# Optimization experiments

Measured on AMD Instinct MI355X. Metric: run time of the kernel, lower is better.

Reference implementation:

```python
import jax, jax.numpy as jnp
import numpy as np

B, D = 16384, 512


def setup_inputs() -> dict:
    key = jax.random.key(0)
    ks = jax.random.split(key, 7)
    s1 = 1.0 / np.sqrt(D + 1)
    s2 = 1.0 / np.sqrt(2 * D + 1)
    return {
        "t": jax.random.uniform(ks[0], (1,), dtype=jnp.float32),
        "z": jax.random.normal(ks[1], (B, D), dtype=jnp.float32),
        "logp_z": jnp.zeros((B, 1), dtype=jnp.float32),
        "W1": jax.random.normal(ks[2], (2 * D, D + 1), dtype=jnp.float32) * s1,
        "b1": jax.random.normal(ks[3], (2 * D,), dtype=jnp.float32) * s1,
        "W2": jax.random.normal(ks[4], (D, 2 * D + 1), dtype=jnp.float32) * s2,
        "b2": jax.random.normal(ks[5], (D,), dtype=jnp.float32) * s2,
    }


def reference(t, z, logp_z, W1, b1, W2, b2):
    # CNF dynamics: dz/dt = fc2(concat(relu(fc1(concat(z, t))), t))
    batch = z.shape[0]
    tt = jnp.full((batch, 1), t[0], dtype=z.dtype)
    x = jnp.concatenate([z, tt], axis=1)            # [B, D+1]
    h_pre = x @ W1.T + b1                           # [B, 2D]
    h = jax.nn.relu(h_pre)
    x2 = jnp.concatenate([h, tt], axis=1)           # [B, 2D+1]
    dz_dt = x2 @ W2.T + b2                          # [B, D]

    # Exact Jacobian trace of linear-relu-linear block (closed form of the
    # per-dim autograd loop in trace_df_dz):
    #   tr J = sum_h relu'(h_pre[:,h]) * (sum_i W2[i,h] * W1[h,i])
    W2h = W2[:, : 2 * D]                            # drop time column, [D, 2D]
    W1z = W1[:, :D]                                 # drop time column, [2D, D]
    c = jnp.sum(W2h.T * W1z, axis=1)                # [2D]
    mask = (h_pre > 0).astype(z.dtype)              # relu'
    trace = mask @ c                                # [B]
    dlogp_z_dt = -trace[:, None]                    # [B, 1]
    return dz_dt, dlogp_z_dt
```

## Files before the change

### kernel.cpp

```cpp
#include <hip/hip_runtime.h>
#include <stdint.h>

#define B_   16384
#define D_   512
#define N1_  1024
#define K1_  512
#define N2_  512
#define K2_  1024

#define DELTA     4e-3f
#define LIST_CAP  (1u << 21)
#define LCAP      1024u

typedef _Float16 f16x8 __attribute__((ext_vector_type(8)));
typedef _Float16 f16x4 __attribute__((ext_vector_type(4)));
typedef float    f32x4 __attribute__((ext_vector_type(4)));

#define MFMA(a, b, c) __builtin_amdgcn_mfma_f32_16x16x32_f16(a, b, c, 0, 0, 0)

__global__ __launch_bounds__(256) void prep_w(
    const float* __restrict__ t,
    const float* __restrict__ W1, const float* __restrict__ b1,
    const float* __restrict__ W2, const float* __restrict__ b2,
    _Float16* __restrict__ wp,
    float* __restrict__ bias1, float* __restrict__ bias2,
    float* __restrict__ cvec, uint32_t* __restrict__ counter) {
  int blk = blockIdx.x, tid = threadIdx.x;
  if (blk < 512) {
    int idx = blk * 256 + tid;
    int g = idx >> 11, rem = idx & 2047;
    int w = rem >> 8, nt = (rem >> 6) & 3, lane = rem & 63;
    int m16 = lane & 15, q = lane >> 4;
    int ch = g >> 5, ph = g & 31;
    const float* src;
    float scale;
    if (ph < 16) {
      int col = ch * 512 + w * 64 + nt * 16 + m16;
      int k = ph * 32 + q * 8;
      src = W1 + (size_t)col * 513 + k;
      scale = 64.f;
    } else {
      int col = w * 64 + nt * 16 + m16;
      int k = ch * 512 + (ph - 16) * 32 + q * 8;
      src = W2 + (size_t)col * 1025 + k;
      scale = 1.f;
    }
    f16x8 hv;
    #pragma unroll
    for (int e = 0; e < 8; ++e) hv[e] = (_Float16)(src[e] * scale);
    *(f16x8*)(wp + (size_t)idx * 8) = hv;
  } else if (blk < 516) {
    int j = (blk - 512) * 256 + tid;
    float t0 = t[0];
    bias1[j] = b1[j] + t0 * W1[(size_t)j * 513 + 512];
    if (j < 512) bias2[j] = b2[j] + t0 * W2[(size_t)j * 1025 + 1024];
    if (j == 0) *counter = 0;
  } else {
    int wave = tid >> 6, lane = tid & 63;
    int j = (blk - 516) * 4 + wave;
    float s = 0.f;
    #pragma unroll
    for (int kk = 0; kk < 8; ++kk) {
      int k = lane + kk * 64;
      s += W2[(size_t)k * 1025 + j] * W1[(size_t)j * 513 + k];
    }
    #pragma unroll
    for (int off = 32; off > 0; off >>= 1) s += __shfl_xor(s, off);
    if (lane == 0) cvec[j] = s;
  }
}


__global__ __launch_bounds__(512) void fused_kernel(
    const float* __restrict__ z, const _Float16* __restrict__ wp,
    const float* __restrict__ bias1, const float* __restrict__ bias2,
    const float* __restrict__ cvec,
    float* __restrict__ out, float* __restrict__ dlogp,
    uint32_t* __restrict__ list, uint32_t* __restrict__ counter) {
  __shared__ __align__(16) _Float16 Az[64 * 512];
  __shared__ __align__(16) _Float16 Hb[64 * 512];
  __shared__ __align__(16) float bias1L[1024];
  __shared__ __align__(16) float cvecL[1024];
  __shared__ uint32_t llist[LCAP];
  __shared__ float redbuf[8][64];
  __shared__ uint32_t lcnt, lbase;

  const int tid  = threadIdx.x;
  const int lane = tid & 63, w = tid >> 6;
  const int q    = lane >> 4, m16 = lane & 15;
  const int sw   = m16 & 7;
  const int bm   = blockIdx.x;

  if (tid == 0) lcnt = 0;

  {
    const float* zp = z + (size_t)bm * 64 * 512;
    #pragma unroll
    for (int i = 0; i < 16; ++i) {
      int slot = i * 512 + tid;
      int row = slot >> 7, u8 = slot & 127;
      f32x4 v = *(const f32x4*)(zp + (size_t)row * 512 + u8 * 4);
      f16x4 hv;
      #pragma unroll
      for (int r = 0; r < 4; ++r) hv[r] = (_Float16)(v[r] * 16.f);
      int gz = (u8 >> 1) ^ (row & 7);
      *(f16x4*)((char*)Az + row * 1024 + gz * 16 + (u8 & 1) * 8) = hv;
    }
  }
  for (int i = tid; i < 1024; i += 512) {
    bias1L[i] = bias1[i];
    cvecL[i]  = cvec[i];
  }
  __syncthreads();

  f32x4 acc1[4][4] = {};
  f32x4 acc2[4][4] = {};
  float tr[4] = {0.f, 0.f, 0.f, 0.f};

  const char* azb   = (const char*)Az + m16 * 1024;
  const char* hbb   = (const char*)Hb + m16 * 1024;
  const char* wbase = (const char*)wp + w * 4096 + lane * 16;

  f16x8 cwA[4], cwB[4];
  #pragma unroll
  for (int nt = 0; nt < 4; ++nt) cwA[nt] = *(const f16x8*)(wbase + nt * 1024);

  for (int ch = 0; ch < 2; ++ch) {
    for (int s2 = 0; s2 < 8; ++s2) {
      const int s = s2 * 2;
      const int g = ch * 32 + s;
      #pragma unroll
      for (int nt = 0; nt < 4; ++nt)
        cwB[nt] = *(const f16x8*)(wbase + (size_t)(g + 1) * 32768 + nt * 1024);
      {
        const int zg = ((s * 4 + q) ^ sw) << 4;
        f16x8 zf0 = *(const f16x8*)(azb + 0 * 16384 + zg);
        f16x8 zf1 = *(const f16x8*)(azb + 1 * 16384 + zg);
        f16x8 zf2 = *(const f16x8*)(azb + 2 * 16384 + zg);
        f16x8 zf3 = *(const f16x8*)(azb + 3 * 16384 + zg);
        __builtin_amdgcn_s_setprio(1);
        #pragma unroll
        for (int nt = 0; nt < 4; ++nt) {
          acc1[0][nt] = MFMA(cwA[nt], zf0, acc1[0][nt]);
          acc1[1][nt] = MFMA(cwA[nt], zf1, acc1[1][nt]);
          acc1[2][nt] = MFMA(cwA[nt], zf2, acc1[2][nt]);
          acc1[3][nt] = MFMA(cwA[nt], zf3, acc1[3][nt]);
        }
        __builtin_amdgcn_s_setprio(0);
      }
      {
        const int gn = (g + 2 > 63) ? 63 : (g + 2);
        #pragma unroll
        for (int nt = 0; nt < 4; ++nt)
          cwA[nt] = *(const f16x8*)(wbase + (size_t)gn * 32768 + nt * 1024);
      }
      {
        const int zg = (((s + 1) * 4 + q) ^ sw) << 4;
        f16x8 zf0 = *(const f16x8*)(azb + 0 * 16384 + zg);
        f16x8 zf1 = *(const f16x8*)(azb + 1 * 16384 + zg);
        f16x8 zf2 = *(const f16x8*)(azb + 2 * 16384 + zg);
        f16x8 zf3 = *(const f16x8*)(azb + 3 * 16384 + zg);
        __builtin_amdgcn_s_setprio(1);
        #pragma unroll
        for (int nt = 0; nt < 4; ++nt) {
          acc1[0][nt] = MFMA(cwB[nt], zf0, acc1[0][nt]);
          acc1[1][nt] = MFMA(cwB[nt], zf1, acc1[1][nt]);
          acc1[2][nt] = MFMA(cwB[nt], zf2, acc1[2][nt]);
          acc1[3][nt] = MFMA(cwB[nt], zf3, acc1[3][nt]);
        }
        __builtin_amdgcn_s_setprio(0);
      }
    }

    __syncthreads();

    #pragma unroll
    for (int nt = 0; nt < 4; ++nt) {
      int colc = w * 64 + nt * 16 + q * 4;
      int col = ch * 512 + colc;
      f32x4 b4 = *(const f32x4*)&bias1L[col];
      f32x4 c4 = *(const f32x4*)&cvecL[col];
      #pragma unroll
      for (int mt = 0; mt < 4; ++mt) {
        int row = mt * 16 + m16;
        f16x4 hv;
        #pragma unroll
        for (int r = 0; r < 4; ++r) {
          float hp = acc1[mt][nt][r] * (1.f / 1024.f) + b4[r];
          hv[r] = (_Float16)(hp > 0.f ? hp : 0.f);
          if (hp > 0.f) tr[mt] += c4[r];
          if (__builtin_fabsf(hp) < DELTA) {
            uint32_t i_ = atomicAdd(&lcnt, 1u);
            if (i_ < LCAP)
              llist[i_] = ((uint32_t)(bm * 64 + row) << 10) | (uint32_t)col | (uint32_t)r |
                          (hp > 0.f ? 0x80000000u : 0u);
          }
        }
        int gg = (colc >> 3) ^ (row & 7);
        *(f16x4*)((char*)Hb + row * 1024 + gg * 16 + (q & 1) * 8) = hv;
        acc1[mt][nt] = (f32x4){0.f, 0.f, 0.f, 0.f};
      }
    }

    __syncthreads();

    for (int t2 = 0; t2 < 8; ++t2) {
      const int t = t2 * 2;
      const int g = ch * 32 + 16 + t;
      #pragma unroll
      for (int nt = 0; nt < 4; ++nt)
        cwB[nt] = *(const f16x8*)(wbase + (size_t)(g + 1) * 32768 + nt * 1024);
      {
        const int hg = ((t * 4 + q) ^ sw) << 4;
        f16x8 hf0 = *(const f16x8*)(hbb + 0 * 16384 + hg);
        f16x8 hf1 = *(const f16x8*)(hbb + 1 * 16384 + hg);
        f16x8 hf2 = *(const f16x8*)(hbb + 2 * 16384 + hg);
        f16x8 hf3 = *(const f16x8*)(hbb + 3 * 16384 + hg);
        __builtin_amdgcn_s_setprio(1);
        #pragma unroll
        for (int nt = 0; nt < 4; ++nt) {
          acc2[0][nt] = MFMA(cwA[nt], hf0, acc2[0][nt]);
          acc2[1][nt] = MFMA(cwA[nt], hf1, acc2[1][nt]);
          acc2[2][nt] = MFMA(cwA[nt], hf2, acc2[2][nt]);
          acc2[3][nt] = MFMA(cwA[nt], hf3, acc2[3][nt]);
        }
        __builtin_amdgcn_s_setprio(0);
      }
      {
        const int gn = (g + 2 > 63) ? 63 : (g + 2);
        #pragma unroll
        for (int nt = 0; nt < 4; ++nt)
          cwA[nt] = *(const f16x8*)(wbase + (size_t)gn * 32768 + nt * 1024);
      }
      {
        const int hg = (((t + 1) * 4 + q) ^ sw) << 4;
        f16x8 hf0 = *(const f16x8*)(hbb + 0 * 16384 + hg);
        f16x8 hf1 = *(const f16x8*)(hbb + 1 * 16384 + hg);
        f16x8 hf2 = *(const f16x8*)(hbb + 2 * 16384 + hg);
        f16x8 hf3 = *(const f16x8*)(hbb + 3 * 16384 + hg);
        __builtin_amdgcn_s_setprio(1);
        #pragma unroll
        for (int nt = 0; nt < 4; ++nt) {
          acc2[0][nt] = MFMA(cwB[nt], hf0, acc2[0][nt]);
          acc2[1][nt] = MFMA(cwB[nt], hf1, acc2[1][nt]);
          acc2[2][nt] = MFMA(cwB[nt], hf2, acc2[2][nt]);
          acc2[3][nt] = MFMA(cwB[nt], hf3, acc2[3][nt]);
        }
        __builtin_amdgcn_s_setprio(0);
      }
    }
  }

  #pragma unroll
  for (int mt = 0; mt < 4; ++mt) {
    int row = bm * 64 + mt * 16 + m16;
    #pragma unroll
    for (int nt = 0; nt < 4; ++nt) {
      int col = w * 64 + nt * 16 + q * 4;
      f32x4 b2v = *(const f32x4*)(bias2 + col);
      *(f32x4*)(out + (size_t)row * 512 + col) = acc2[mt][nt] + b2v;
    }
  }

  #pragma unroll
  for (int mt = 0; mt < 4; ++mt) {
    tr[mt] += __shfl_xor(tr[mt], 16);
    tr[mt] += __shfl_xor(tr[mt], 32);
  }
  if (q == 0) {
    #pragma unroll
    for (int mt = 0; mt < 4; ++mt) redbuf[w][mt * 16 + m16] = tr[mt];
  }
  __syncthreads();
  if (tid < 64) {
    float s = 0.f;
    #pragma unroll
    for (int ww = 0; ww < 8; ++ww) s += redbuf[ww][tid];
    dlogp[bm * 64 + tid] = -s;
  }

  if (tid == 0) {
    uint32_t n = lcnt < LCAP ? lcnt : LCAP;
    lbase = atomicAdd(counter, n);
  }
  __syncthreads();
  uint32_t n = lcnt < LCAP ? lcnt : LCAP;
  uint32_t base = lbase;
  for (uint32_t i = tid; i < n; i += 512) {
    uint32_t gi = base + i;
    if (gi < LIST_CAP) list[gi] = llist[i];
  }
}

__global__ __launch_bounds__(256)
void fixup_kernel(const float* __restrict__ z, const float* __restrict__ W1,
                  const float* __restrict__ bias1, const float* __restrict__ cvec,
                  const uint32_t* __restrict__ list, const uint32_t* __restrict__ counter,
                  float* __restrict__ dlogp) {
  uint32_t cnt = *counter;
  if (cnt > LIST_CAP) cnt = LIST_CAP;
  const int wid = (blockIdx.x * 256 + threadIdx.x) >> 6;
  const int lane = threadIdx.x & 63;
  const int nw = gridDim.x * 4;
  for (uint32_t i = wid; i < cnt; i += nw) {
    uint32_t e = list[i];
    int row = (int)((e >> 10) & 16383u);
    int col = (int)(e & 1023u);
    int oldm = (int)(e >> 31);
    float s = 0.f;
    #pragma unroll
    for (int it = 0; it < 8; ++it) {
      int k = it * 64 + lane;
      s += z[(size_t)row * 512 + k] * W1[(size_t)col * 513 + k];
    }
    #pragma unroll
    for (int off = 32; off > 0; off >>= 1) s += __shfl_xor(s, off);
    if (lane == 0) {
      float hp = s + bias1[col];
      int newm = hp > 0.f ? 1 : 0;
      if (newm != oldm)
        atomicAdd(&dlogp[row], oldm ? cvec[col] : -cvec[col]);
    }
  }
}

extern "C" void kernel_launch(void* const* d_in, const int* in_sizes, int n_in,
                              void* d_out, int out_size, void* d_ws, size_t ws_size,
                              hipStream_t stream) {
  const float* t  = (const float*)d_in[0];
  const float* z  = (const float*)d_in[1];
  const float* W1 = (const float*)d_in[3];
  const float* b1 = (const float*)d_in[4];
  const float* W2 = (const float*)d_in[5];
  const float* b2 = (const float*)d_in[6];

  float* out   = (float*)d_out;
  float* dlogp = out + (size_t)B_ * D_;

  char* ws = (char*)d_ws;
  _Float16* wp    = (_Float16*)ws; ws += (size_t)64 * 32768;
  float*    bias1 = (float*)ws;    ws += 1024 * 4;
  float*    bias2 = (float*)ws;    ws += 512 * 4;
  float*    cvec  = (float*)ws;    ws += 1024 * 4;
  uint32_t* counter = (uint32_t*)ws; ws += 256;
  uint32_t* list  = (uint32_t*)ws; ws += (size_t)LIST_CAP * 4;

  prep_w<<<772, 256, 0, stream>>>(t, W1, b1, W2, b2, wp, bias1, bias2, cvec, counter);
  fused_kernel<<<256, 512, 0, stream>>>(z, wp, bias1, bias2, cvec, out, dlogp, list, counter);
  fixup_kernel<<<2048, 256, 0, stream>>>(z, W1, bias1, cvec, list, counter, dlogp);
}
```

Measured before the change: 159.5 us.

## Fold near-zero mask fixup into fused kernel, drop global list and fixup launch

Near-threshold relu mask corrections are now recomputed in fp32 inside the fused kernel, using each block's shared-memory list and accumulating into a shared per-row buffer before writing dlogp. This removes the global counter, the global list writes and the separate fixup kernel launch with its global atomics. In exchange, each block does its own fixup work serially after the GEMMs, and load across blocks may be uneven.

```diff
diff --git a/kernel.cpp b/kernel.cpp
--- a/kernel.cpp
+++ b/kernel.cpp
@@ -9,7 +9,6 @@
 #define K2_  1024
 
 #define DELTA     4e-3f
-#define LIST_CAP  (1u << 21)
 #define LCAP      1024u
 
 typedef _Float16 f16x8 __attribute__((ext_vector_type(8)));
@@ -24,7 +23,7 @@
     const float* __restrict__ W2, const float* __restrict__ b2,
     _Float16* __restrict__ wp,
     float* __restrict__ bias1, float* __restrict__ bias2,
-    float* __restrict__ cvec, uint32_t* __restrict__ counter) {
+    float* __restrict__ cvec) {
   int blk = blockIdx.x, tid = threadIdx.x;
   if (blk < 512) {
     int idx = blk * 256 + tid;
@@ -54,7 +53,6 @@
     float t0 = t[0];
     bias1[j] = b1[j] + t0 * W1[(size_t)j * 513 + 512];
     if (j < 512) bias2[j] = b2[j] + t0 * W2[(size_t)j * 1025 + 1024];
-    if (j == 0) *counter = 0;
   } else {
     int wave = tid >> 6, lane = tid & 63;
     int j = (blk - 516) * 4 + wave;
@@ -73,17 +71,18 @@
 
 __global__ __launch_bounds__(512) void fused_kernel(
     const float* __restrict__ z, const _Float16* __restrict__ wp,
+    const float* __restrict__ W1f,
     const float* __restrict__ bias1, const float* __restrict__ bias2,
     const float* __restrict__ cvec,
-    float* __restrict__ out, float* __restrict__ dlogp,
-    uint32_t* __restrict__ list, uint32_t* __restrict__ counter) {
+    float* __restrict__ out, float* __restrict__ dlogp) {
   __shared__ __align__(16) _Float16 Az[64 * 512];
   __shared__ __align__(16) _Float16 Hb[64 * 512];
   __shared__ __align__(16) float bias1L[1024];
   __shared__ __align__(16) float cvecL[1024];
   __shared__ uint32_t llist[LCAP];
   __shared__ float redbuf[8][64];
-  __shared__ uint32_t lcnt, lbase;
+  __shared__ float fixv[64];
+  __shared__ uint32_t lcnt;
 
   const int tid  = threadIdx.x;
   const int lane = tid & 63, w = tid >> 6;
@@ -92,6 +91,7 @@
   const int bm   = blockIdx.x;
 
   if (tid == 0) lcnt = 0;
+  if (tid < 64) fixv[tid] = 0.f;
 
   {
     const float* zp = z + (size_t)bm * 64 * 512;
@@ -192,7 +192,7 @@
           if (__builtin_fabsf(hp) < DELTA) {
             uint32_t i_ = atomicAdd(&lcnt, 1u);
             if (i_ < LCAP)
-              llist[i_] = ((uint32_t)(bm * 64 + row) << 10) | (uint32_t)col | (uint32_t)r |
+              llist[i_] = ((uint32_t)row << 10) | (uint32_t)(col + r) |
                           (hp > 0.f ? 0x80000000u : 0u);
           }
         }
@@ -272,55 +272,39 @@
     for (int mt = 0; mt < 4; ++mt) redbuf[w][mt * 16 + m16] = tr[mt];
   }
   __syncthreads();
+
+  {
+    uint32_t n = lcnt < LCAP ? lcnt : LCAP;
+    for (uint32_t i = w; i < n; i += 8) {
+      uint32_t e = llist[i];
+      int row  = (int)((e >> 10) & 63u);
+      int col  = (int)(e & 1023u);
+      int oldm = (int)(e >> 31);
+      const float* zr = z   + ((size_t)(bm * 64 + row)) * 512;
+      const float* wc = W1f + (size_t)col * 513;
+      float s = 0.f;
+      #pragma unroll
+      for (int it = 0; it < 8; ++it) {
+        int k = it * 64 + lane;
+        s += zr[k] * wc[k];
+      }
+      #pragma unroll
+      for (int off = 32; off > 0; off >>= 1) s += __shfl_xor(s, off);
+      if (lane == 0) {
+        float hp = s + bias1L[col];
+        int newm = hp > 0.f ? 1 : 0;
+        if (newm != oldm)
+          atomicAdd(&fixv[row], oldm ? cvecL[col] : -cvecL[col]);
+      }
+    }
+  }
+  __syncthreads();
+
   if (tid < 64) {
     float s = 0.f;
     #pragma unroll
     for (int ww = 0; ww < 8; ++ww) s += redbuf[ww][tid];
-    dlogp[bm * 64 + tid] = -s;
-  }
-
-  if (tid == 0) {
-    uint32_t n = lcnt < LCAP ? lcnt : LCAP;
-    lbase = atomicAdd(counter, n);
-  }
-  __syncthreads();
-  uint32_t n = lcnt < LCAP ? lcnt : LCAP;
-  uint32_t base = lbase;
-  for (uint32_t i = tid; i < n; i += 512) {
-    uint32_t gi = base + i;
-    if (gi < LIST_CAP) list[gi] = llist[i];
-  }
-}
-
-__global__ __launch_bounds__(256)
-void fixup_kernel(const float* __restrict__ z, const float* __restrict__ W1,
-                  const float* __restrict__ bias1, const float* __restrict__ cvec,
-                  const uint32_t* __restrict__ list, const uint32_t* __restrict__ counter,
-                  float* __restrict__ dlogp) {
-  uint32_t cnt = *counter;
-  if (cnt > LIST_CAP) cnt = LIST_CAP;
-  const int wid = (blockIdx.x * 256 + threadIdx.x) >> 6;
-  const int lane = threadIdx.x & 63;
-  const int nw = gridDim.x * 4;
-  for (uint32_t i = wid; i < cnt; i += nw) {
-    uint32_t e = list[i];
-    int row = (int)((e >> 10) & 16383u);
-    int col = (int)(e & 1023u);
-    int oldm = (int)(e >> 31);
-    float s = 0.f;
-    #pragma unroll
-    for (int it = 0; it < 8; ++it) {
-      int k = it * 64 + lane;
-      s += z[(size_t)row * 512 + k] * W1[(size_t)col * 513 + k];
-    }
-    #pragma unroll
-    for (int off = 32; off > 0; off >>= 1) s += __shfl_xor(s, off);
-    if (lane == 0) {
-      float hp = s + bias1[col];
-      int newm = hp > 0.f ? 1 : 0;
-      if (newm != oldm)
-        atomicAdd(&dlogp[row], oldm ? cvec[col] : -cvec[col]);
-    }
+    dlogp[bm * 64 + tid] = -s + fixv[tid];
   }
 }
 
@@ -342,10 +326,7 @@
   float*    bias1 = (float*)ws;    ws += 1024 * 4;
   float*    bias2 = (float*)ws;    ws += 512 * 4;
   float*    cvec  = (float*)ws;    ws += 1024 * 4;
-  uint32_t* counter = (uint32_t*)ws; ws += 256;
-  uint32_t* list  = (uint32_t*)ws; ws += (size_t)LIST_CAP * 4;
-
-  prep_w<<<772, 256, 0, stream>>>(t, W1, b1, W2, b2, wp, bias1, bias2, cvec, counter);
-  fused_kernel<<<256, 512, 0, stream>>>(z, wp, bias1, bias2, cvec, out, dlogp, list, counter);
-  fixup_kernel<<<2048, 256, 0, stream>>>(z, W1, bias1, cvec, list, counter, dlogp);
+
+  prep_w<<<772, 256, 0, stream>>>(t, W1, b1, W2, b2, wp, bias1, bias2, cvec);
+  fused_kernel<<<256, 512, 0, stream>>>(z, wp, W1, bias1, bias2, cvec, out, dlogp);
 }
```

After: 152.1 us. 1.05x faster.
